# Performance work log

Hardware: AMD Instinct MI355X
Metric: run time of the kernel (lower is better)

Reference implementation:

```python
import jax, jax.numpy as jnp
import numpy as np

NQ = 4   # num_qubits (CNOT chain in source hardcodes wires 0..3)
NL = 1   # num_layers
B = 1048576

# CNOT as rank-4 tensor [c_out, t_out, c_in, t_in]
_CNOT = jnp.asarray(
    np.array([[1, 0, 0, 0],
              [0, 1, 0, 0],
              [0, 0, 0, 1],
              [0, 0, 1, 0]], dtype=np.complex64).reshape(2, 2, 2, 2))


def _rz(t):
    e = jnp.exp(-0.5j * t.astype(jnp.complex64))
    z = jnp.zeros_like(e)
    return jnp.stack([jnp.stack([e, z]), jnp.stack([z, jnp.conj(e)])])


def _ry(t):
    c = jnp.cos(0.5 * t).astype(jnp.complex64)
    s = jnp.sin(0.5 * t).astype(jnp.complex64)
    return jnp.stack([jnp.stack([c, -s]), jnp.stack([s, c])])


def _u3(th, ph, lm):
    c = jnp.cos(0.5 * th).astype(jnp.complex64)
    s = jnp.sin(0.5 * th).astype(jnp.complex64)
    eph = jnp.exp(1j * ph.astype(jnp.complex64))
    elm = jnp.exp(1j * lm.astype(jnp.complex64))
    return jnp.stack([jnp.stack([c, -elm * s]),
                      jnp.stack([eph * s, eph * elm * c])])


def _apply_1q(state, U, q):
    s = jnp.tensordot(U, state, axes=([1], [q]))
    return jnp.moveaxis(s, 0, q)


def _apply_2q(state, U, c, t):
    s = jnp.tensordot(U, state, axes=([2, 3], [c, t]))
    return jnp.moveaxis(s, (0, 1), (c, t))


def _circuit(enc, w):
    # H on all qubits applied to |0...0> -> uniform real amplitude 2^{-NQ/2}
    state = jnp.full((2,) * NQ, 2.0 ** (-NQ / 2), dtype=jnp.complex64)
    # per-qubit encoding: RZ, RY, RZ
    for q in range(NQ):
        state = _apply_1q(state, _rz(enc[q, 0]), q)
        state = _apply_1q(state, _ry(enc[q, 1]), q)
        state = _apply_1q(state, _rz(enc[q, 2]), q)
    for l in range(NL):
        for (c, t) in ((0, 1), (1, 2), (2, 3), (3, 0)):
            state = _apply_2q(state, _CNOT, c, t)
        for q in range(NQ):
            state = _apply_1q(state, _u3(w[l, q, 0], w[l, q, 1], w[l, q, 2]), q)
    probs = jnp.real(state * jnp.conj(state))
    zs = []
    for q in range(NQ):
        p = probs.sum(axis=tuple(i for i in range(NQ) if i != q))  # (2,)
        zs.append(p[0] - p[1])
    return jnp.stack(zs)  # (NQ,)


def setup_inputs() -> dict:
    key = jax.random.key(0)
    k1, k2 = jax.random.split(key)
    enc_angles = jax.random.normal(k1, (B, NQ, 3), dtype=jnp.float32)
    weights = jax.random.normal(k2, (NL, NQ, 3), dtype=jnp.float32)
    return {"enc_angles": enc_angles, "weights": weights}


def reference(enc_angles, weights):
    out = jax.vmap(lambda e: _circuit(e, weights))(enc_angles)  # (B, NQ)
    return out.astype(jnp.float32)
```

## Files before the change

kernel.cpp:

```cpp
#include <hip/hip_runtime.h>


__global__ void vqc_prep(const float* __restrict__ w, float* __restrict__ mz) {
    int q = threadIdx.x;
    if (q >= 4) return;
    float th = w[q * 3 + 0];
    float lm = w[q * 3 + 2];
    float s, c, sl, cl;
    sincosf(0.5f * th, &s, &c);
    sincosf(lm, &sl, &cl);
    mz[q * 4 + 0] = c * c - s * s;
    mz[q * 4 + 1] = -4.0f * c * s * cl;
    mz[q * 4 + 2] = -4.0f * c * s * sl;
    mz[q * 4 + 3] = 0.0f;
}

__global__ __launch_bounds__(256) void vqc_main(const float4* __restrict__ enc,
                                                const float4* __restrict__ mz,
                                                float4* __restrict__ out, int B) {
    int b = blockIdx.x * blockDim.x + threadIdx.x;
    if (b >= B) return;

    float4 e0 = enc[b * 3 + 0];
    float4 e1 = enc[b * 3 + 1];
    float4 e2 = enc[b * 3 + 2];
    float4 m0 = mz[0], m1 = mz[1], m2 = mz[2], m3 = mz[3];

    float ang[12] = {e0.x, e0.y, e0.z, e0.w, e1.x, e1.y, e1.z, e1.w,
                     e2.x, e2.y, e2.z, e2.w};

    float vx[4][2], vy[4][2];
    const float inv = 0.70710678118654752f;
#pragma unroll
    for (int q = 0; q < 4; ++q) {
        float sa, ca, sb, cb, sg, cg;
        __sincosf(0.5f * ang[3 * q + 0], &sa, &ca);
        __sincosf(0.5f * ang[3 * q + 1], &sb, &cb);
        __sincosf(0.5f * ang[3 * q + 2], &sg, &cg);
        float P = cb - sb, Q = cb + sb;
        float y0x = ca * P * inv, y0y = -sa * Q * inv;
        float y1x = ca * Q * inv, y1y = sa * P * inv;
        vx[q][0] = cg * y0x + sg * y0y;
        vy[q][0] = cg * y0y - sg * y0x;
        vx[q][1] = cg * y1x - sg * y1y;
        vy[q][1] = cg * y1y + sg * y1x;
    }

    float ux[4], uy[4], wx[4], wy[4];
#pragma unroll
    for (int i = 0; i < 2; ++i)
#pragma unroll
        for (int j = 0; j < 2; ++j) {
            ux[i * 2 + j] = vx[0][i] * vx[1][j] - vy[0][i] * vy[1][j];
            uy[i * 2 + j] = vx[0][i] * vy[1][j] + vy[0][i] * vx[1][j];
            wx[i * 2 + j] = vx[2][i] * vx[3][j] - vy[2][i] * vy[3][j];
            wy[i * 2 + j] = vx[2][i] * vy[3][j] + vy[2][i] * vx[3][j];
        }

    float ax[16], ay[16];
#pragma unroll
    for (int h = 0; h < 4; ++h)
#pragma unroll
        for (int l = 0; l < 4; ++l) {
            ax[h * 4 + l] = ux[h] * wx[l] - uy[h] * wy[l];
            ay[h * 4 + l] = ux[h] * wy[l] + uy[h] * wx[l];
        }

    const int cm[4] = {8, 4, 2, 1};
    const int tm[4] = {4, 2, 1, 8};
#pragma unroll
    for (int k = 0; k < 4; ++k) {
#pragma unroll
        for (int i = 0; i < 16; ++i) {
            if ((i & cm[k]) && !(i & tm[k])) {
                int j = i | tm[k];
                float tx = ax[i], ty = ay[i];
                ax[i] = ax[j]; ay[i] = ay[j];
                ax[j] = tx;    ay[j] = ty;
            }
        }
    }

    float p[16];
#pragma unroll
    for (int i = 0; i < 16; ++i) p[i] = ax[i] * ax[i] + ay[i] * ay[i];

    float al[4] = {m0.x, m1.x, m2.x, m3.x};
    float g1[4] = {m0.y, m1.y, m2.y, m3.y};
    float g2[4] = {m0.z, m1.z, m2.z, m3.z};

    float z[4];
#pragma unroll
    for (int q = 0; q < 4; ++q) {
        int m = 8 >> q;
        float acc = 0.0f;
#pragma unroll
        for (int i = 0; i < 16; ++i) {
            if (!(i & m)) {
                int j = i | m;
                float cx = ax[i] * ax[j] + ay[i] * ay[j];
                float cy = ay[i] * ax[j] - ax[i] * ay[j];
                acc += al[q] * (p[i] - p[j]) + g1[q] * cx + g2[q] * cy;
            }
        }
        z[q] = acc;
    }

    out[b] = make_float4(z[0], z[1], z[2], z[3]);
}

extern "C" void kernel_launch(void* const* d_in, const int* in_sizes, int n_in,
                              void* d_out, int out_size, void* d_ws, size_t ws_size,
                              hipStream_t stream) {
    const float* enc = (const float*)d_in[0];
    const float* w   = (const float*)d_in[1];
    float* out = (float*)d_out;
    float* mz  = (float*)d_ws;

    int B = in_sizes[0] / 12;

    vqc_prep<<<1, 64, 0, stream>>>(w, mz);
    int grid = (B + 255) / 256;
    vqc_main<<<grid, 256, 0, stream>>>((const float4*)enc, (const float4*)mz,
                                       (float4*)out, B);
}
```

Before: 93.68 us.

## Replace statevector simulation with closed-form Bloch-vector expectation formulas

Drops the per-thread 16-amplitude statevector, CNOT permutation and pairwise reduction. Each qubit's encoded state now becomes a Bloch vector (x, y, z), and the four outputs are computed as short products of those components weighted by the U3 parameters. The separate prep kernel is folded into the main kernel, which has four threads compute the weight terms into shared memory followed by a __syncthreads. This cuts arithmetic and register pressure sharply, though the kernel is likely memory-bound, and it relies on the closed form being exactly right for this fixed circuit.

```diff
diff --git a/kernel.cpp b/kernel.cpp
--- a/kernel.cpp
+++ b/kernel.cpp
@@ -1,112 +1,63 @@
 #include <hip/hip_runtime.h>
 
 
-__global__ void vqc_prep(const float* __restrict__ w, float* __restrict__ mz) {
-    int q = threadIdx.x;
-    if (q >= 4) return;
-    float th = w[q * 3 + 0];
-    float lm = w[q * 3 + 2];
-    float s, c, sl, cl;
-    sincosf(0.5f * th, &s, &c);
-    sincosf(lm, &sl, &cl);
-    mz[q * 4 + 0] = c * c - s * s;
-    mz[q * 4 + 1] = -4.0f * c * s * cl;
-    mz[q * 4 + 2] = -4.0f * c * s * sl;
-    mz[q * 4 + 3] = 0.0f;
-}
+__global__ __launch_bounds__(256) void vqc_main(const float4* __restrict__ enc,
+                                                const float* __restrict__ w,
+                                                float4* __restrict__ out, int B) {
+    __shared__ float wal[4], wA[4], wB[4];
+    const int t = threadIdx.x;
+    const int b = blockIdx.x * blockDim.x + t;
 
-__global__ __launch_bounds__(256) void vqc_main(const float4* __restrict__ enc,
-                                                const float4* __restrict__ mz,
-                                                float4* __restrict__ out, int B) {
-    int b = blockIdx.x * blockDim.x + threadIdx.x;
-    if (b >= B) return;
+    if (t < 4) {
+        float th = w[t * 3 + 0];
+        float lm = w[t * 3 + 2];
+        float st, ct, sl, cl;
+        __sincosf(th, &st, &ct);
+        __sincosf(lm, &sl, &cl);
+        wal[t] = ct;
+        wA[t] = -st * cl;
+        wB[t] = st * sl;
+    }
 
-    float4 e0 = enc[b * 3 + 0];
-    float4 e1 = enc[b * 3 + 1];
-    float4 e2 = enc[b * 3 + 2];
-    float4 m0 = mz[0], m1 = mz[1], m2 = mz[2], m3 = mz[3];
+    const bool live = (b < B);
+    float4 e0, e1, e2;
+    if (live) {
+        e0 = enc[b * 3 + 0];
+        e1 = enc[b * 3 + 1];
+        e2 = enc[b * 3 + 2];
+    }
+    __syncthreads();
+    if (!live) return;
 
-    float ang[12] = {e0.x, e0.y, e0.z, e0.w, e1.x, e1.y, e1.z, e1.w,
-                     e2.x, e2.y, e2.z, e2.w};
+    const float ang[12] = {e0.x, e0.y, e0.z, e0.w, e1.x, e1.y, e1.z, e1.w,
+                           e2.x, e2.y, e2.z, e2.w};
 
-    float vx[4][2], vy[4][2];
-    const float inv = 0.70710678118654752f;
+    float x[4], y[4], z[4];
 #pragma unroll
     for (int q = 0; q < 4; ++q) {
         float sa, ca, sb, cb, sg, cg;
-        __sincosf(0.5f * ang[3 * q + 0], &sa, &ca);
-        __sincosf(0.5f * ang[3 * q + 1], &sb, &cb);
-        __sincosf(0.5f * ang[3 * q + 2], &sg, &cg);
-        float P = cb - sb, Q = cb + sb;
-        float y0x = ca * P * inv, y0y = -sa * Q * inv;
-        float y1x = ca * Q * inv, y1y = sa * P * inv;
-        vx[q][0] = cg * y0x + sg * y0y;
-        vy[q][0] = cg * y0y - sg * y0x;
-        vx[q][1] = cg * y1x - sg * y1y;
-        vy[q][1] = cg * y1y + sg * y1x;
+        __sincosf(ang[3 * q + 0], &sa, &ca);
+        __sincosf(ang[3 * q + 1], &sb, &cb);
+        __sincosf(ang[3 * q + 2], &sg, &cg);
+        float cc = ca * cb;
+        x[q] = cc * cg - sa * sg;
+        y[q] = cc * sg + sa * cg;
+        z[q] = -ca * sb;
     }
 
-    float ux[4], uy[4], wx[4], wy[4];
-#pragma unroll
-    for (int i = 0; i < 2; ++i)
-#pragma unroll
-        for (int j = 0; j < 2; ++j) {
-            ux[i * 2 + j] = vx[0][i] * vx[1][j] - vy[0][i] * vy[1][j];
-            uy[i * 2 + j] = vx[0][i] * vy[1][j] + vy[0][i] * vx[1][j];
-            wx[i * 2 + j] = vx[2][i] * vx[3][j] - vy[2][i] * vy[3][j];
-            wy[i * 2 + j] = vx[2][i] * vy[3][j] + vy[2][i] * vx[3][j];
-        }
+    const float z23   = z[2] * z[3];
+    const float z123  = z[1] * z23;
+    const float z01   = z[0] * z[1];
+    const float z012  = z01 * z[2];
+    const float z0123 = z012 * z[3];
+    const float x01   = x[0] * x[1];
 
-    float ax[16], ay[16];
-#pragma unroll
-    for (int h = 0; h < 4; ++h)
-#pragma unroll
-        for (int l = 0; l < 4; ++l) {
-            ax[h * 4 + l] = ux[h] * wx[l] - uy[h] * wy[l];
-            ay[h * 4 + l] = ux[h] * wy[l] + uy[h] * wx[l];
-        }
+    const float o0 = wal[0] * z123  + wA[0] * x01           + wB[0] * (x[0] * (y[1] * z23));
+    const float o1 = wal[1] * z01   + wA[1] * (x[1] * x[2]) + wB[1] * ((z[0] * y[1]) * x[2]);
+    const float o2 = wal[2] * z012  + wA[2] * (x[2] * x[3]) + wB[2] * ((z01 * y[2]) * x[3]);
+    const float o3 = wal[3] * z0123 + wA[3] * (x01 * x[3])  - wB[3] * (((y[0] * y[1]) * z[2]) * y[3]);
 
-    const int cm[4] = {8, 4, 2, 1};
-    const int tm[4] = {4, 2, 1, 8};
-#pragma unroll
-    for (int k = 0; k < 4; ++k) {
-#pragma unroll
-        for (int i = 0; i < 16; ++i) {
-            if ((i & cm[k]) && !(i & tm[k])) {
-                int j = i | tm[k];
-                float tx = ax[i], ty = ay[i];
-                ax[i] = ax[j]; ay[i] = ay[j];
-                ax[j] = tx;    ay[j] = ty;
-            }
-        }
-    }
-
-    float p[16];
-#pragma unroll
-    for (int i = 0; i < 16; ++i) p[i] = ax[i] * ax[i] + ay[i] * ay[i];
-
-    float al[4] = {m0.x, m1.x, m2.x, m3.x};
-    float g1[4] = {m0.y, m1.y, m2.y, m3.y};
-    float g2[4] = {m0.z, m1.z, m2.z, m3.z};
-
-    float z[4];
-#pragma unroll
-    for (int q = 0; q < 4; ++q) {
-        int m = 8 >> q;
-        float acc = 0.0f;
-#pragma unroll
-        for (int i = 0; i < 16; ++i) {
-            if (!(i & m)) {
-                int j = i | m;
-                float cx = ax[i] * ax[j] + ay[i] * ay[j];
-                float cy = ay[i] * ax[j] - ax[i] * ay[j];
-                acc += al[q] * (p[i] - p[j]) + g1[q] * cx + g2[q] * cy;
-            }
-        }
-        z[q] = acc;
-    }
-
-    out[b] = make_float4(z[0], z[1], z[2], z[3]);
+    out[b] = make_float4(o0, o1, o2, o3);
 }
 
 extern "C" void kernel_launch(void* const* d_in, const int* in_sizes, int n_in,
@@ -115,12 +66,9 @@
     const float* enc = (const float*)d_in[0];
     const float* w   = (const float*)d_in[1];
     float* out = (float*)d_out;
-    float* mz  = (float*)d_ws;
+    (void)d_ws; (void)ws_size;
 
     int B = in_sizes[0] / 12;
-
-    vqc_prep<<<1, 64, 0, stream>>>(w, mz);
     int grid = (B + 255) / 256;
-    vqc_main<<<grid, 256, 0, stream>>>((const float4*)enc, (const float4*)mz,
-                                       (float4*)out, B);
+    vqc_main<<<grid, 256, 0, stream>>>((const float4*)enc, w, (float4*)out, B);
 }
```

After: 85.53 us. 1.1x faster.
